# Performance work log

Measured on AMD Instinct MI355X. Metric: run time of the kernel, lower is better.

## Reference

```python
import jax, jax.numpy as jnp
import numpy as np
import math

B, N, D, O, H = 8, 1024, 512, 512, 8
HD = O // H  # head_dim = 64


def setup_inputs() -> dict:
    key = jax.random.key(0)
    ks = jax.random.split(key, 12)
    x = jax.random.normal(ks[0], (B, N, D), dtype=jnp.float32)
    adj = jax.random.uniform(ks[1], (B, N, N), dtype=jnp.float32)  # unused by forward math
    mask = jax.random.randint(ks[2], (B, N), 0, 2) > 0  # bool padding mask
    # learned params (torch nn.Linear: y = x @ W.T + b)
    qkv_w = jax.random.normal(ks[3], (3 * O, D), dtype=jnp.float32) / math.sqrt(D)
    qkv_b = jnp.zeros((3 * O,), dtype=jnp.float32)
    # self_loop_W: 1/head_dim + U(0,1), per head, non-trainable
    self_loop_W = (1.0 / HD + jax.random.uniform(ks[4], (1, H, 1, 1))).astype(jnp.float32)
    w1 = jax.random.normal(ks[5], (O, O), dtype=jnp.float32) / math.sqrt(O)
    b1 = jnp.zeros((O,), dtype=jnp.float32)
    w2 = jax.random.normal(ks[6], (O, O), dtype=jnp.float32) / math.sqrt(O)
    b2 = jnp.zeros((O,), dtype=jnp.float32)
    wr = jax.random.normal(ks[7], (O, D), dtype=jnp.float32) / math.sqrt(D)
    br = jnp.zeros((O,), dtype=jnp.float32)
    return {"x": x, "adj": adj, "mask": mask, "self_loop_W": self_loop_W,
            "qkv_w": qkv_w, "qkv_b": qkv_b, "w1": w1, "b1": b1,
            "w2": w2, "b2": b2, "wr": wr, "br": br}


def reference(x, adj, mask, self_loop_W, qkv_w, qkv_b, w1, b1, w2, b2, wr, br):
    fmask = mask.astype(x.dtype)  # [B,N]
    # --- MoireAttention ---
    qkv = x @ qkv_w.T + qkv_b                       # [B,N,3O]
    qkv = qkv.reshape(B, N, 3, H, HD).transpose(2, 0, 3, 1, 4)  # [3,B,H,N,hd]
    Q, K, V = qkv[0], qkv[1], qkv[2]
    scores = jnp.einsum('bhnd,bhmd->bhnm', Q, K) / math.sqrt(HD)  # [B,H,N,N]
    eye = jnp.eye(N, dtype=scores.dtype)
    scores = scores + eye[None, None] * self_loop_W  # per-head diagonal self-loop bias
    mask2d = mask[:, None, :, None] & mask[:, None, None, :]  # [B,1,N,N]
    scores = jnp.where(mask2d, scores, jnp.asarray(-1e6, scores.dtype))
    attn = jax.nn.softmax(scores, axis=-1)
    h = jnp.einsum('bhnm,bhmd->bhnd', attn, V)      # [B,H,N,hd]
    h = h.transpose(0, 2, 1, 3).reshape(B, N, O)
    # --- mask, FFN (eval mode: noise/dropout are identity), mask ---
    h = h * fmask[..., None]
    h = jax.nn.relu(h @ w1.T + b1) @ w2.T + b2
    h = h * fmask[..., None]
    # --- residual blend ---
    x_proj = x @ wr.T + br
    return h * 0.5 + x_proj * 0.5
```

## Files before the change

### kernel.cpp

```cpp
#include <hip/hip_runtime.h>
#include <hip/hip_bf16.h>

typedef __attribute__((ext_vector_type(8))) short short8;
typedef __attribute__((ext_vector_type(4))) float f32x4;
typedef __attribute__((ext_vector_type(4))) short short4v;

#define BB 8
#define NN 1024
#define DD 512
#define OO 512
#define HH 8
#define HD 64
#define MM (BB * NN)

#define QSC 0.18033688f
#define KSHIFT -11.54156032f
#define KMASKED -30000.0f

__device__ __forceinline__ void gload_lds16(const void* g, void* l) {
  __builtin_amdgcn_global_load_lds(
      (const __attribute__((address_space(1))) void*)g,
      (__attribute__((address_space(3))) void*)l, 16, 0, 0);
}

__device__ __forceinline__ uint2 cvt4(float4 v) {
  union { uint2 u; __hip_bfloat16 h[4]; } t;
  t.h[0] = __float2bfloat16(v.x);
  t.h[1] = __float2bfloat16(v.y);
  t.h[2] = __float2bfloat16(v.z);
  t.h[3] = __float2bfloat16(v.w);
  return t.u;
}

#define SEG_N 10
struct ConvArgs {
  const float* src[SEG_N];
  __hip_bfloat16* dst[SEG_N];
  int n4[SEG_N];
};

__global__ void convert_kernel(ConvArgs a) {
  const int t = blockIdx.y;
  const int n4 = a.n4[t];
  const float4* fs = (const float4*)a.src[t];
  uint2* d = (uint2*)a.dst[t];
  for (int i = blockIdx.x * blockDim.x + threadIdx.x; i < n4;
       i += gridDim.x * blockDim.x)
    d[i] = cvt4(fs[i]);
}

__global__ __launch_bounds__(256) void gemm_qkv(
    const __hip_bfloat16* __restrict__ A0, const __hip_bfloat16* __restrict__ B0,
    const __hip_bfloat16* __restrict__ bias0, const __hip_bfloat16* __restrict__ bias1,
    __hip_bfloat16* __restrict__ out0, __hip_bfloat16* __restrict__ out1,
    __hip_bfloat16* __restrict__ out2, float* __restrict__ outf, int Kd) {
  __shared__ __align__(16) __hip_bfloat16 smem[8192];
  __hip_bfloat16* As = smem;
  __hip_bfloat16* Bs = smem + 4096;

  const int tid  = threadIdx.x;
  const int wave = tid >> 6;
  const int lane = tid & 63;
  const int fl   = lane & 15;
  const int fk   = (lane >> 4) * 8;
  const int wm   = (wave & 1) * 64;
  const int wn   = (wave >> 1) * 64;
  const int bid     = blockIdx.x;
  const int rowpart = 8 * (bid & 7) + ((bid >> 3) & 7);
  const int colpart = bid >> 6;
  const int m0 = rowpart * 128;
  const int n0 = colpart * 128;
  const int glr  = lane >> 2;
  const int glc  = (lane & 3) * 8;

  f32x4 acc[4][4];
#pragma unroll
  for (int i = 0; i < 4; ++i)
#pragma unroll
    for (int j = 0; j < 4; ++j) acc[i][j] = (f32x4){0.f, 0.f, 0.f, 0.f};

  char* lb = (char*)smem;
  for (int k0 = 0; k0 < Kd; k0 += 32) {
    __syncthreads();
    gload_lds16(A0 + (size_t)(m0 + wave * 16 + glr) * Kd + k0 + glc,
                lb + wave * 1024 + lane * 16);
    gload_lds16(A0 + (size_t)(m0 + 64 + wave * 16 + glr) * Kd + k0 + glc,
                lb + (wave + 4) * 1024 + lane * 16);
    gload_lds16(B0 + (size_t)(n0 + wave * 16 + glr) * Kd + k0 + glc,
                lb + 8192 + wave * 1024 + lane * 16);
    gload_lds16(B0 + (size_t)(n0 + 64 + wave * 16 + glr) * Kd + k0 + glc,
                lb + 8192 + (wave + 4) * 1024 + lane * 16);
    __syncthreads();

    short8 af[4], bfr[4];
#pragma unroll
    for (int i = 0; i < 4; ++i)
      af[i] = *(const short8*)&As[(wm + i * 16 + fl) * 32 + fk];
#pragma unroll
    for (int j = 0; j < 4; ++j)
      bfr[j] = *(const short8*)&Bs[(wn + j * 16 + fl) * 32 + fk];
#pragma unroll
    for (int i = 0; i < 4; ++i)
#pragma unroll
      for (int j = 0; j < 4; ++j)
        acc[i][j] = __builtin_amdgcn_mfma_f32_16x16x32_bf16(af[i], bfr[j],
                                                            acc[i][j], 0, 0, 0);
  }

  const int rb = (lane >> 4) * 4;
  const int part = n0 >> 9;
  if (part < 2) {
    __hip_bfloat16* dst = (part == 0) ? out0 : out1;
    const float scf = (part == 0) ? QSC : 1.0f;
#pragma unroll
    for (int j = 0; j < 4; ++j) {
      const int colb  = n0 + wn + j * 16;
      const int o     = colb & 511;
      const int headq = o >> 6;
      const int d     = (o & 63) + fl;
      const float bi  = __bfloat162float(bias0[colb + fl]);
#pragma unroll
      for (int i = 0; i < 4; ++i) {
#pragma unroll
        for (int r = 0; r < 4; ++r) {
          const int row = m0 + wm + i * 16 + rb + r;
          const int bb  = row >> 10;
          const int nn  = row & 1023;
          dst[((size_t)((bb << 3) + headq) * NN + nn) * HD + d] =
              __float2bfloat16((acc[i][j][r] + bi) * scf);
        }
      }
    }
  } else if (part == 2) {
    __syncthreads();
    __hip_bfloat16* tsc = smem + wave * 1120;
    const int bb  = (m0 + wm) >> 10;
    const int nnb = (m0 + wm) & 1023;
    const int dl  = lane >> 2;
    const int cc  = (lane & 3) * 16;
#pragma unroll
    for (int j = 0; j < 4; ++j) {
      const int colb  = n0 + wn + j * 16;
      const int o     = colb & 511;
      const int headq = o >> 6;
      const int dbase = o & 63;
      const float bi  = __bfloat162float(bias0[colb + fl]);
#pragma unroll
      for (int i = 0; i < 4; ++i) {
#pragma unroll
        for (int r = 0; r < 4; ++r) {
          const int rr = i * 16 + rb + r;
          tsc[fl * 70 + rr] = __float2bfloat16(acc[i][j][r] + bi);
        }
      }
      uint4 r0 = *(const uint4*)&tsc[dl * 70 + cc];
      uint4 r1 = *(const uint4*)&tsc[dl * 70 + cc + 8];
      __hip_bfloat16* vdst =
          out2 + ((size_t)((bb << 3) + headq) * HD + dbase + dl) * NN + nnb;
      *(uint4*)&vdst[cc] = r0;
      *(uint4*)&vdst[cc + 8] = r1;
    }
  } else {
#pragma unroll
    for (int j = 0; j < 4; ++j) {
      const int colb = n0 + wn + j * 16;
      const int o    = colb & 511;
      const float bi = 0.5f * __bfloat162float(bias1[o + fl]);
#pragma unroll
      for (int i = 0; i < 4; ++i) {
#pragma unroll
        for (int r = 0; r < 4; ++r) {
          const int row = m0 + wm + i * 16 + rb + r;
          outf[(size_t)row * OO + o + fl] = 0.5f * acc[i][j][r] + bi;
        }
      }
    }
  }
}

__global__ __launch_bounds__(1024) void ffn_fused(
    const __hip_bfloat16* __restrict__ hb,
    const __hip_bfloat16* __restrict__ w1, const __hip_bfloat16* __restrict__ w2,
    const __hip_bfloat16* __restrict__ b1, const __hip_bfloat16* __restrict__ b2,
    const int* __restrict__ mask, float* __restrict__ outf) {
  __shared__ __align__(16) __hip_bfloat16 h1s[32 * 520];
  __shared__ float Mrow[32];

  const int tid  = threadIdx.x;
  const int wv   = tid >> 6;
  const int lane = tid & 63;
  const int fl   = lane & 15;
  const int quad = lane >> 4;
  const int fk   = quad * 8;
  const int m0   = blockIdx.x * 32;

  {
    const int col = (tid & 63) * 8;
#pragma unroll
    for (int c = 0; c < 2; ++c) {
      const int row = c * 16 + (tid >> 6);
      *(uint4*)&h1s[row * 520 + col] =
          *(const uint4*)&hb[(size_t)(m0 + row) * OO + col];
    }
    if (tid < 32) Mrow[tid] = (mask[m0 + tid] != 0) ? 1.f : 0.f;
  }
  __syncthreads();

  f32x4 acc[2][2];

  auto run_phase = [&](const __hip_bfloat16* __restrict__ W) {
    const __hip_bfloat16* wl0 = W + (size_t)(wv * 32 + fl) * 512 + fk;
    short8 a[4][2];
#pragma unroll
    for (int d = 0; d < 4; ++d)
#pragma unroll
      for (int j = 0; j < 2; ++j)
        a[d][j] = *(const short8*)(wl0 + d * 32 + j * 8192);
#pragma unroll
    for (int k = 0; k < 16; ++k) {
      short8 bh_[2];
#pragma unroll
      for (int i = 0; i < 2; ++i)
        bh_[i] = *(const short8*)&h1s[(i * 16 + fl) * 520 + k * 32 + fk];
      __builtin_amdgcn_s_setprio(1);
#pragma unroll
      for (int j = 0; j < 2; ++j)
#pragma unroll
        for (int i = 0; i < 2; ++i)
          acc[i][j] = __builtin_amdgcn_mfma_f32_16x16x32_bf16(a[k & 3][j], bh_[i],
                                                              acc[i][j], 0, 0, 0);
      __builtin_amdgcn_s_setprio(0);
      if (k < 12) {
#pragma unroll
        for (int j = 0; j < 2; ++j)
          a[k & 3][j] = *(const short8*)(wl0 + (k + 4) * 32 + j * 8192);
      }
      __builtin_amdgcn_sched_barrier(0);
    }
  };

#pragma unroll
  for (int i = 0; i < 2; ++i)
#pragma unroll
    for (int j = 0; j < 2; ++j) acc[i][j] = (f32x4){0.f, 0.f, 0.f, 0.f};
  run_phase(w1);
  __syncthreads();

#pragma unroll
  for (int j = 0; j < 2; ++j) {
    const int c0 = wv * 32 + j * 16 + quad * 4;
    union { short4v s; __hip_bfloat16 h[4]; } bv;
    bv.s = *(const short4v*)&b1[c0];
#pragma unroll
    for (int i = 0; i < 2; ++i) {
      const float mr = Mrow[i * 16 + fl];
      union { short4v s; __hip_bfloat16 h[4]; } pu;
#pragma unroll
      for (int e = 0; e < 4; ++e) {
        const float v = fmaxf(acc[i][j][e] + __bfloat162float(bv.h[e]), 0.f) * mr;
        pu.h[e] = __float2bfloat16(v);
      }
      *(short4v*)&h1s[(i * 16 + fl) * 520 + c0] = pu.s;
    }
  }
  __syncthreads();

#pragma unroll
  for (int i = 0; i < 2; ++i)
#pragma unroll
    for (int j = 0; j < 2; ++j) acc[i][j] = (f32x4){0.f, 0.f, 0.f, 0.f};
  run_phase(w2);

#pragma unroll
  for (int j = 0; j < 2; ++j) {
    const int c0 = wv * 32 + j * 16 + quad * 4;
    union { short4v s; __hip_bfloat16 h[4]; } b2v;
    b2v.s = *(const short4v*)&b2[c0];
#pragma unroll
    for (int i = 0; i < 2; ++i) {
      const float mr = Mrow[i * 16 + fl];
      const int row = m0 + i * 16 + fl;
      float4 prev = *(const float4*)&outf[(size_t)row * OO + c0];
      float4 o;
      o.x = prev.x + 0.5f * (acc[i][j][0] + mr * __bfloat162float(b2v.h[0]));
      o.y = prev.y + 0.5f * (acc[i][j][1] + mr * __bfloat162float(b2v.h[1]));
      o.z = prev.z + 0.5f * (acc[i][j][2] + mr * __bfloat162float(b2v.h[2]));
      o.w = prev.w + 0.5f * (acc[i][j][3] + mr * __bfloat162float(b2v.h[3]));
      *(float4*)&outf[(size_t)row * OO + c0] = o;
    }
  }
}

__global__ __launch_bounds__(512) void attn_kernel(
    const __hip_bfloat16* __restrict__ Qb, const __hip_bfloat16* __restrict__ Kb,
    const __hip_bfloat16* __restrict__ Vt, const __hip_bfloat16* __restrict__ slw,
    const int* __restrict__ mask, __hip_bfloat16* __restrict__ hb) {
  __shared__ __align__(16) __hip_bfloat16 QPs[128 * 72];
  __shared__ __align__(16) __hip_bfloat16 Ks[2][64 * 72];
  __shared__ __align__(16) __hip_bfloat16 Vs[2][64 * 72];
  __shared__ float Msf[NN];

  const int tid  = threadIdx.x;
  const int wave = tid >> 6;
  const int lane = tid & 63;
  const int fl   = lane & 15;
  const int quad = lane >> 4;
  const int fk   = quad * 8;
  const int rb   = quad * 4;
  const int bh   = blockIdx.x & 63;
  const int qblk = blockIdx.x >> 6;
  const int b    = bh >> 3;
  const int head = bh & 7;
  const int q0   = qblk * 128;

  const float slwL2 = __bfloat162float(slw[head]) * 1.44269504f;

  const int srow2 = tid >> 3;
  const int sc2   = (tid & 7) * 8;
  const __hip_bfloat16* kgb = Kb + (size_t)bh * NN * HD;
  const __hip_bfloat16* vgb = Vt + (size_t)bh * HD * NN;

  uint4 kr = *(const uint4*)(kgb + (size_t)srow2 * HD + sc2);
  uint4 vr = *(const uint4*)(vgb + (size_t)srow2 * NN + sc2);
  {
    const int srow = tid >> 2;
    const int sc   = (tid & 3) * 16;
    const __hip_bfloat16* qg = Qb + ((size_t)bh * NN + q0) * HD;
    uint4 v0 = *(const uint4*)(qg + srow * HD + sc);
    uint4 v1 = *(const uint4*)(qg + srow * HD + sc + 8);
    *(uint4*)&QPs[srow * 72 + sc] = v0;
    *(uint4*)&QPs[srow * 72 + sc + 8] = v1;
#pragma unroll
    for (int k = 0; k < 2; ++k) {
      const int idx = tid * 2 + k;
      Msf[idx] = (mask[b * NN + idx] != 0) ? KSHIFT : KMASKED;
    }
  }
  *(uint4*)&Ks[0][srow2 * 72 + sc2] = kr;
  *(uint4*)&Vs[0][srow2 * 72 + sc2] = vr;
  kr = *(const uint4*)(kgb + (size_t)(64 + srow2) * HD + sc2);
  vr = *(const uint4*)(vgb + (size_t)srow2 * NN + 64 + sc2);
  __syncthreads();
  const short8 qa0 = *(const short8*)&QPs[(wave * 16 + fl) * 72 + fk];
  const short8 qa1 = *(const short8*)&QPs[(wave * 16 + fl) * 72 + fk + 32];

  float lsum = 0.f;
  f32x4 Oacc[4];
#pragma unroll
  for (int t = 0; t < 4; ++t) Oacc[t] = (f32x4){0.f, 0.f, 0.f, 0.f};

  const int kbdiag = 2 * qblk + (wave >> 2);

  for (int kb = 0; kb < NN / 64; ++kb) {
    const int kbase = kb * 64;
    const int cur   = kb & 1;
    const __hip_bfloat16* Kc = Ks[cur];
    const __hip_bfloat16* Vc = Vs[cur];

    f32x4 sfr[4];
    __builtin_amdgcn_s_setprio(1);
#pragma unroll
    for (int j = 0; j < 4; ++j) {
      const short8 kf0 = *(const short8*)&Kc[(j * 16 + fl) * 72 + fk];
      const short8 kf1 = *(const short8*)&Kc[(j * 16 + fl) * 72 + fk + 32];
      f32x4 z = (f32x4){0.f, 0.f, 0.f, 0.f};
      z = __builtin_amdgcn_mfma_f32_16x16x32_bf16(kf0, qa0, z, 0, 0, 0);
      z = __builtin_amdgcn_mfma_f32_16x16x32_bf16(kf1, qa1, z, 0, 0, 0);
      sfr[j] = z;
    }
    __builtin_amdgcn_s_setprio(0);

    if (kb == kbdiag) {
      if ((fl >> 2) == quad) sfr[wave & 3][fl & 3] += slwL2;
    }

#pragma unroll
    for (int j = 0; j < 4; ++j) {
      const f32x4 mb4 = *(const f32x4*)&Msf[kbase + j * 16 + quad * 4];
      union { short4v s; __hip_bfloat16 h[4]; } pu;
      float ps = 0.f;
#pragma unroll
      for (int e = 0; e < 4; ++e) {
        const float pv = exp2f(sfr[j][e] + mb4[e]);
        ps += pv;
        pu.h[e] = __float2bfloat16(pv);
      }
      lsum += ps;
      *(short4v*)&QPs[(wave * 16 + fl) * 72 + j * 16 + quad * 4] = pu.s;
    }

    const short8 pa0 = *(const short8*)&QPs[(wave * 16 + fl) * 72 + fk];
    const short8 pa1 = *(const short8*)&QPs[(wave * 16 + fl) * 72 + fk + 32];
    __builtin_amdgcn_s_setprio(1);
#pragma unroll
    for (int t = 0; t < 4; ++t) {
      const short8 vf0 = *(const short8*)&Vc[(t * 16 + fl) * 72 + fk];
      const short8 vf1 = *(const short8*)&Vc[(t * 16 + fl) * 72 + fk + 32];
      Oacc[t] = __builtin_amdgcn_mfma_f32_16x16x32_bf16(pa0, vf0, Oacc[t], 0, 0, 0);
      Oacc[t] = __builtin_amdgcn_mfma_f32_16x16x32_bf16(pa1, vf1, Oacc[t], 0, 0, 0);
    }
    __builtin_amdgcn_s_setprio(0);

    if (kb + 1 < NN / 64) {
      *(uint4*)&Ks[cur ^ 1][srow2 * 72 + sc2] = kr;
      *(uint4*)&Vs[cur ^ 1][srow2 * 72 + sc2] = vr;
      if (kb + 2 < NN / 64) {
        const int nk = kbase + 128;
        kr = *(const uint4*)(kgb + (size_t)(nk + srow2) * HD + sc2);
        vr = *(const uint4*)(vgb + (size_t)srow2 * NN + nk + sc2);
      }
      __builtin_amdgcn_sched_barrier(0);
      __syncthreads();
    }
  }

  float l = lsum;
  l += __shfl_xor(l, 16, 64);
  l += __shfl_xor(l, 32, 64);
  const int qrow_me = q0 + wave * 16 + fl;
  const float qm = (mask[b * NN + qrow_me] != 0) ? 1.f : 0.f;
  const float sf = qm / fmaxf(l, 1e-30f);

  float scl[4];
#pragma unroll
  for (int r = 0; r < 4; ++r) scl[r] = __shfl(sf, rb + r, 64);

#pragma unroll
  for (int t = 0; t < 4; ++t) {
    const int d = t * 16 + fl;
#pragma unroll
    for (int r = 0; r < 4; ++r) {
      const int qrow_g = q0 + wave * 16 + rb + r;
      hb[(size_t)(b * NN + qrow_g) * OO + head * HD + d] =
          __float2bfloat16(Oacc[t][r] * scl[r]);
    }
  }
}

extern "C" void kernel_launch(void* const* d_in, const int* in_sizes, int n_in,
                              void* d_out, int out_size, void* d_ws, size_t ws_size,
                              hipStream_t stream) {
  const float* x_raw    = (const float*)d_in[0];
  const int* mask       = (const int*)d_in[2];
  const float* slw_raw  = (const float*)d_in[3];
  const float* qkvw_raw = (const float*)d_in[4];
  const float* qkvb_raw = (const float*)d_in[5];
  const float* w1_raw   = (const float*)d_in[6];
  const float* b1_raw   = (const float*)d_in[7];
  const float* w2_raw   = (const float*)d_in[8];
  const float* b2_raw   = (const float*)d_in[9];
  const float* wr_raw   = (const float*)d_in[10];
  const float* br_raw   = (const float*)d_in[11];
  float* outf           = (float*)d_out;

  __hip_bfloat16* p = (__hip_bfloat16*)d_ws;
  __hip_bfloat16* xc    = p; p += (size_t)MM * DD;
  __hip_bfloat16* qkvwc = p; p += 3 * OO * DD;
  __hip_bfloat16* wrc   = p; p += OO * DD;
  __hip_bfloat16* w1c   = p; p += OO * OO;
  __hip_bfloat16* w2c   = p; p += OO * OO;
  __hip_bfloat16* qkvbc = p; p += 3 * OO;
  __hip_bfloat16* b1c   = p; p += OO;
  __hip_bfloat16* b2c   = p; p += OO;
  __hip_bfloat16* brc   = p; p += OO;
  __hip_bfloat16* slwc  = p; p += 64;
  const size_t ebuf = (size_t)BB * HH * NN * HD;
  __hip_bfloat16* Qb = p; p += ebuf;
  __hip_bfloat16* Kb = p; p += ebuf;
  __hip_bfloat16* Vb = p; p += ebuf;
  __hip_bfloat16* hb = p; p += ebuf;

  if (ws_size < (size_t)((char*)p - (char*)d_ws)) return;

  ConvArgs ca;
  ca.src[0] = x_raw;    ca.dst[0] = xc;    ca.n4[0] = MM * DD / 4;
  ca.src[1] = qkvw_raw; ca.dst[1] = qkvwc; ca.n4[1] = 3 * OO * DD / 4;
  ca.src[2] = w1_raw;   ca.dst[2] = w1c;   ca.n4[2] = OO * OO / 4;
  ca.src[3] = w2_raw;   ca.dst[3] = w2c;   ca.n4[3] = OO * OO / 4;
  ca.src[4] = wr_raw;   ca.dst[4] = wrc;   ca.n4[4] = OO * DD / 4;
  ca.src[5] = qkvb_raw; ca.dst[5] = qkvbc; ca.n4[5] = 3 * OO / 4;
  ca.src[6] = b1_raw;   ca.dst[6] = b1c;   ca.n4[6] = OO / 4;
  ca.src[7] = b2_raw;   ca.dst[7] = b2c;   ca.n4[7] = OO / 4;
  ca.src[8] = br_raw;   ca.dst[8] = brc;   ca.n4[8] = OO / 4;
  ca.src[9] = slw_raw;  ca.dst[9] = slwc;  ca.n4[9] = HH / 4;
  convert_kernel<<<dim3(1024, SEG_N), 256, 0, stream>>>(ca);

  gemm_qkv<<<1024, 256, 0, stream>>>(xc, qkvwc, qkvbc, brc, Qb, Kb, Vb, outf, DD);
  attn_kernel<<<BB * HH * (NN / 128), 512, 0, stream>>>(Qb, Kb, Vb, slwc, mask, hb);
  ffn_fused<<<256, 1024, 0, stream>>>(hb, w1c, w2c, b1c, b2c, mask, outf);
}
```

Measured before the change: 211.0 us.

## Process 256 query rows per attention block, two 16-row tiles per wave

Each attention block now covers 256 query rows instead of 128, and each wave handles two 16-row Q tiles that share the same K/V fragments loaded from LDS. This halves the K/V global and LDS traffic per query row and halves the grid to 256 blocks. In exchange it raises register and LDS use per block, and the smaller grid may leave some of the 256 compute units less well balanced. The diagonal self-loop handling is generalised to both tiles.

```diff
diff --git a/kernel.cpp b/kernel.cpp
--- a/kernel.cpp
+++ b/kernel.cpp
@@ -295,7 +295,7 @@
     const __hip_bfloat16* __restrict__ Qb, const __hip_bfloat16* __restrict__ Kb,
     const __hip_bfloat16* __restrict__ Vt, const __hip_bfloat16* __restrict__ slw,
     const int* __restrict__ mask, __hip_bfloat16* __restrict__ hb) {
-  __shared__ __align__(16) __hip_bfloat16 QPs[128 * 72];
+  __shared__ __align__(16) __hip_bfloat16 QPs[256 * 72];
   __shared__ __align__(16) __hip_bfloat16 Ks[2][64 * 72];
   __shared__ __align__(16) __hip_bfloat16 Vs[2][64 * 72];
   __shared__ float Msf[NN];
@@ -311,9 +311,15 @@
   const int qblk = blockIdx.x >> 6;
   const int b    = bh >> 3;
   const int head = bh & 7;
-  const int q0   = qblk * 128;
+  const int q0   = qblk * 256;
 
   const float slwL2 = __bfloat162float(slw[head]) * 1.44269504f;
+
+  const int twf  = 2 * wave;
+  const int kbdA = 4 * qblk + (twf >> 2);
+  const int jdA  = twf & 3;
+  const int kbdB = 4 * qblk + ((twf + 1) >> 2);
+  const int jdB  = (twf + 1) & 3;
 
   const int srow2 = tid >> 3;
   const int sc2   = (tid & 7) * 8;
@@ -323,13 +329,17 @@
   uint4 kr = *(const uint4*)(kgb + (size_t)srow2 * HD + sc2);
   uint4 vr = *(const uint4*)(vgb + (size_t)srow2 * NN + sc2);
   {
-    const int srow = tid >> 2;
-    const int sc   = (tid & 3) * 16;
-    const __hip_bfloat16* qg = Qb + ((size_t)bh * NN + q0) * HD;
-    uint4 v0 = *(const uint4*)(qg + srow * HD + sc);
-    uint4 v1 = *(const uint4*)(qg + srow * HD + sc + 8);
-    *(uint4*)&QPs[srow * 72 + sc] = v0;
-    *(uint4*)&QPs[srow * 72 + sc + 8] = v1;
+    const int qr = tid >> 1;
+    const int qc = (tid & 1) * 32;
+    const __hip_bfloat16* qg = Qb + ((size_t)bh * NN + q0 + qr) * HD + qc;
+    uint4 v0 = *(const uint4*)(qg);
+    uint4 v1 = *(const uint4*)(qg + 8);
+    uint4 v2 = *(const uint4*)(qg + 16);
+    uint4 v3 = *(const uint4*)(qg + 24);
+    *(uint4*)&QPs[qr * 72 + qc] = v0;
+    *(uint4*)&QPs[qr * 72 + qc + 8] = v1;
+    *(uint4*)&QPs[qr * 72 + qc + 16] = v2;
+    *(uint4*)&QPs[qr * 72 + qc + 24] = v3;
 #pragma unroll
     for (int k = 0; k < 2; ++k) {
       const int idx = tid * 2 + k;
@@ -341,15 +351,18 @@
   kr = *(const uint4*)(kgb + (size_t)(64 + srow2) * HD + sc2);
   vr = *(const uint4*)(vgb + (size_t)srow2 * NN + 64 + sc2);
   __syncthreads();
-  const short8 qa0 = *(const short8*)&QPs[(wave * 16 + fl) * 72 + fk];
-  const short8 qa1 = *(const short8*)&QPs[(wave * 16 + fl) * 72 + fk + 32];
-
-  float lsum = 0.f;
-  f32x4 Oacc[4];
-#pragma unroll
-  for (int t = 0; t < 4; ++t) Oacc[t] = (f32x4){0.f, 0.f, 0.f, 0.f};
-
-  const int kbdiag = 2 * qblk + (wave >> 2);
+  const short8 qa0A = *(const short8*)&QPs[(wave * 32 + fl) * 72 + fk];
+  const short8 qa1A = *(const short8*)&QPs[(wave * 32 + fl) * 72 + fk + 32];
+  const short8 qa0B = *(const short8*)&QPs[(wave * 32 + 16 + fl) * 72 + fk];
+  const short8 qa1B = *(const short8*)&QPs[(wave * 32 + 16 + fl) * 72 + fk + 32];
+
+  float lsumA = 0.f, lsumB = 0.f;
+  f32x4 OaccA[4], OaccB[4];
+#pragma unroll
+  for (int t = 0; t < 4; ++t) {
+    OaccA[t] = (f32x4){0.f, 0.f, 0.f, 0.f};
+    OaccB[t] = (f32x4){0.f, 0.f, 0.f, 0.f};
+  }
 
   for (int kb = 0; kb < NN / 64; ++kb) {
     const int kbase = kb * 64;
@@ -357,47 +370,67 @@
     const __hip_bfloat16* Kc = Ks[cur];
     const __hip_bfloat16* Vc = Vs[cur];
 
-    f32x4 sfr[4];
+    f32x4 sfrA[4], sfrB[4];
     __builtin_amdgcn_s_setprio(1);
 #pragma unroll
     for (int j = 0; j < 4; ++j) {
       const short8 kf0 = *(const short8*)&Kc[(j * 16 + fl) * 72 + fk];
       const short8 kf1 = *(const short8*)&Kc[(j * 16 + fl) * 72 + fk + 32];
-      f32x4 z = (f32x4){0.f, 0.f, 0.f, 0.f};
-      z = __builtin_amdgcn_mfma_f32_16x16x32_bf16(kf0, qa0, z, 0, 0, 0);
-      z = __builtin_amdgcn_mfma_f32_16x16x32_bf16(kf1, qa1, z, 0, 0, 0);
-      sfr[j] = z;
+      f32x4 zA = (f32x4){0.f, 0.f, 0.f, 0.f};
+      zA = __builtin_amdgcn_mfma_f32_16x16x32_bf16(kf0, qa0A, zA, 0, 0, 0);
+      zA = __builtin_amdgcn_mfma_f32_16x16x32_bf16(kf1, qa1A, zA, 0, 0, 0);
+      sfrA[j] = zA;
+      f32x4 zB = (f32x4){0.f, 0.f, 0.f, 0.f};
+      zB = __builtin_amdgcn_mfma_f32_16x16x32_bf16(kf0, qa0B, zB, 0, 0, 0);
+      zB = __builtin_amdgcn_mfma_f32_16x16x32_bf16(kf1, qa1B, zB, 0, 0, 0);
+      sfrB[j] = zB;
     }
     __builtin_amdgcn_s_setprio(0);
 
-    if (kb == kbdiag) {
-      if ((fl >> 2) == quad) sfr[wave & 3][fl & 3] += slwL2;
+    if ((fl >> 2) == quad && (kb == kbdA || kb == kbdB)) {
+#pragma unroll
+      for (int j = 0; j < 4; ++j)
+#pragma unroll
+        for (int e = 0; e < 4; ++e)
+          if ((fl & 3) == e) {
+            if (kb == kbdA && j == jdA) sfrA[j][e] += slwL2;
+            if (kb == kbdB && j == jdB) sfrB[j][e] += slwL2;
+          }
     }
 
 #pragma unroll
     for (int j = 0; j < 4; ++j) {
       const f32x4 mb4 = *(const f32x4*)&Msf[kbase + j * 16 + quad * 4];
-      union { short4v s; __hip_bfloat16 h[4]; } pu;
-      float ps = 0.f;
+      union { short4v s; __hip_bfloat16 h[4]; } puA, puB;
+      float psA = 0.f, psB = 0.f;
 #pragma unroll
       for (int e = 0; e < 4; ++e) {
-        const float pv = exp2f(sfr[j][e] + mb4[e]);
-        ps += pv;
-        pu.h[e] = __float2bfloat16(pv);
-      }
-      lsum += ps;
-      *(short4v*)&QPs[(wave * 16 + fl) * 72 + j * 16 + quad * 4] = pu.s;
-    }
-
-    const short8 pa0 = *(const short8*)&QPs[(wave * 16 + fl) * 72 + fk];
-    const short8 pa1 = *(const short8*)&QPs[(wave * 16 + fl) * 72 + fk + 32];
+        const float pvA = exp2f(sfrA[j][e] + mb4[e]);
+        psA += pvA;
+        puA.h[e] = __float2bfloat16(pvA);
+        const float pvB = exp2f(sfrB[j][e] + mb4[e]);
+        psB += pvB;
+        puB.h[e] = __float2bfloat16(pvB);
+      }
+      lsumA += psA;
+      lsumB += psB;
+      *(short4v*)&QPs[(wave * 32 + fl) * 72 + j * 16 + quad * 4] = puA.s;
+      *(short4v*)&QPs[(wave * 32 + 16 + fl) * 72 + j * 16 + quad * 4] = puB.s;
+    }
+
+    const short8 paA0 = *(const short8*)&QPs[(wave * 32 + fl) * 72 + fk];
+    const short8 paA1 = *(const short8*)&QPs[(wave * 32 + fl) * 72 + fk + 32];
+    const short8 paB0 = *(const short8*)&QPs[(wave * 32 + 16 + fl) * 72 + fk];
+    const short8 paB1 = *(const short8*)&QPs[(wave * 32 + 16 + fl) * 72 + fk + 32];
     __builtin_amdgcn_s_setprio(1);
 #pragma unroll
     for (int t = 0; t < 4; ++t) {
       const short8 vf0 = *(const short8*)&Vc[(t * 16 + fl) * 72 + fk];
       const short8 vf1 = *(const short8*)&Vc[(t * 16 + fl) * 72 + fk + 32];
-      Oacc[t] = __builtin_amdgcn_mfma_f32_16x16x32_bf16(pa0, vf0, Oacc[t], 0, 0, 0);
-      Oacc[t] = __builtin_amdgcn_mfma_f32_16x16x32_bf16(pa1, vf1, Oacc[t], 0, 0, 0);
+      OaccA[t] = __builtin_amdgcn_mfma_f32_16x16x32_bf16(paA0, vf0, OaccA[t], 0, 0, 0);
+      OaccA[t] = __builtin_amdgcn_mfma_f32_16x16x32_bf16(paA1, vf1, OaccA[t], 0, 0, 0);
+      OaccB[t] = __builtin_amdgcn_mfma_f32_16x16x32_bf16(paB0, vf0, OaccB[t], 0, 0, 0);
+      OaccB[t] = __builtin_amdgcn_mfma_f32_16x16x32_bf16(paB1, vf1, OaccB[t], 0, 0, 0);
     }
     __builtin_amdgcn_s_setprio(0);
 
@@ -414,25 +447,27 @@
     }
   }
 
-  float l = lsum;
-  l += __shfl_xor(l, 16, 64);
-  l += __shfl_xor(l, 32, 64);
-  const int qrow_me = q0 + wave * 16 + fl;
-  const float qm = (mask[b * NN + qrow_me] != 0) ? 1.f : 0.f;
-  const float sf = qm / fmaxf(l, 1e-30f);
-
-  float scl[4];
-#pragma unroll
-  for (int r = 0; r < 4; ++r) scl[r] = __shfl(sf, rb + r, 64);
-
-#pragma unroll
-  for (int t = 0; t < 4; ++t) {
-    const int d = t * 16 + fl;
-#pragma unroll
-    for (int r = 0; r < 4; ++r) {
-      const int qrow_g = q0 + wave * 16 + rb + r;
-      hb[(size_t)(b * NN + qrow_g) * OO + head * HD + d] =
-          __float2bfloat16(Oacc[t][r] * scl[r]);
+#pragma unroll
+  for (int f = 0; f < 2; ++f) {
+    float l = (f == 0) ? lsumA : lsumB;
+    l += __shfl_xor(l, 16, 64);
+    l += __shfl_xor(l, 32, 64);
+    const int qrow_me = q0 + wave * 32 + f * 16 + fl;
+    const float qm = (mask[b * NN + qrow_me] != 0) ? 1.f : 0.f;
+    const float sf = qm / fmaxf(l, 1e-30f);
+    float scl[4];
+#pragma unroll
+    for (int r = 0; r < 4; ++r) scl[r] = __shfl(sf, rb + r, 64);
+#pragma unroll
+    for (int t = 0; t < 4; ++t) {
+      const int d = t * 16 + fl;
+#pragma unroll
+      for (int r = 0; r < 4; ++r) {
+        const int qrow_g = q0 + wave * 32 + f * 16 + rb + r;
+        const float ov = (f == 0) ? OaccA[t][r] : OaccB[t][r];
+        hb[(size_t)(b * NN + qrow_g) * OO + head * HD + d] =
+            __float2bfloat16(ov * scl[r]);
+      }
     }
   }
 }
@@ -486,6 +521,6 @@
   convert_kernel<<<dim3(1024, SEG_N), 256, 0, stream>>>(ca);
 
   gemm_qkv<<<1024, 256, 0, stream>>>(xc, qkvwc, qkvbc, brc, Qb, Kb, Vb, outf, DD);
-  attn_kernel<<<BB * HH * (NN / 128), 512, 0, stream>>>(Qb, Kb, Vb, slwc, mask, hb);
+  attn_kernel<<<BB * HH * (NN / 256), 512, 0, stream>>>(Qb, Kb, Vb, slwc, mask, hb);
   ffn_fused<<<256, 1024, 0, stream>>>(hb, w1c, w2c, b1c, b2c, mask, outf);
 }
```

Result: no change. 210.3 us (-0.3%).
